# Performance work log

Measured on AMD Instinct MI355X. Metric: run time of the kernel, lower is better.

Reference implementation:

```python
import jax, jax.numpy as jnp
import numpy as np

B_SZ = 32; CTX = 8192; NP = 512; P = 16          # batch, context, n_patches, patch_size
DM = 1024; DS = 16; DC = 4; EXP = 2               # d_model, d_state, d_conv, expand
DI = EXP * DM                                     # d_inner = 2048
DTR = DM // 16                                    # dt_rank = 64


def _ln(x, g, b, eps=1e-5):
    m = x.mean(-1, keepdims=True)
    v = ((x - m) ** 2).mean(-1, keepdims=True)
    return (x - m) / jnp.sqrt(v + eps) * g + b


def _posemb_sincos_1d(n, d, temperature=10000.0):
    pos = jnp.arange(n, dtype=jnp.float32)
    omega = jnp.arange(d // 2, dtype=jnp.float32) / (d // 2 - 1)
    omega = 1.0 / (temperature ** omega)
    ang = pos[:, None] * omega[None, :]            # [n, d/2]
    return jnp.concatenate([jnp.sin(ang), jnp.cos(ang)], axis=1)  # [n, d]


def setup_inputs() -> dict:
    key = jax.random.key(0)
    ks = jax.random.split(key, 10)
    s = lambda k, shape, scale: jax.random.normal(k, shape, jnp.float32) * scale
    return {
        "x": jax.random.normal(ks[0], (B_SZ, CTX), jnp.float32),
        # patch embedding: LN(patch) -> Linear(P, DM) -> LN(DM)
        "ln1_g": jnp.ones((P,), jnp.float32), "ln1_b": jnp.zeros((P,), jnp.float32),
        "Wp": s(ks[1], (P, DM), P ** -0.5), "bp": jnp.zeros((DM,), jnp.float32),
        "ln2_g": jnp.ones((DM,), jnp.float32), "ln2_b": jnp.zeros((DM,), jnp.float32),
        # Mamba block params (mamba-ssm conventions: in_proj/out_proj bias=False, conv bias=True)
        "W_in": s(ks[2], (DM, 2 * DI), DM ** -0.5),
        "conv_w": s(ks[3], (DI, DC), DC ** -0.5), "conv_b": jnp.zeros((DI,), jnp.float32),
        "W_x": s(ks[4], (DI, DTR + 2 * DS), DI ** -0.5),
        "W_dt": s(ks[5], (DTR, DI), DTR ** -0.5),
        "b_dt": jnp.full((DI,), -4.6, jnp.float32),  # softplus(b_dt) ~ 0.01 (typical dt init)
        "A_log": jnp.log(jnp.broadcast_to(jnp.arange(1, DS + 1, dtype=jnp.float32), (DI, DS))),
        "D": jnp.ones((DI,), jnp.float32),
        "W_out": s(ks[6], (DI, DM), DI ** -0.5),
        "ln3_g": jnp.ones((DM,), jnp.float32), "ln3_b": jnp.zeros((DM,), jnp.float32),
        "Wh": s(ks[7], (DM, 1), DM ** -0.5), "bh": jnp.zeros((1,), jnp.float32),
    }


def reference(x, ln1_g, ln1_b, Wp, bp, ln2_g, ln2_b, W_in, conv_w, conv_b,
              W_x, W_dt, b_dt, A_log, D, W_out, ln3_g, ln3_b, Wh, bh):
    B = x.shape[0]
    # --- patch embedding: 'b 1 (n p) -> b n p' (c=1), LN, Linear, LN ---
    patches = x.reshape(B, NP, P)
    h = _ln(patches, ln1_g, ln1_b)
    h = h @ Wp + bp
    h = _ln(h, ln2_g, ln2_b)                        # [B, NP, DM]
    h = h + _posemb_sincos_1d(NP, DM)
    # --- Mamba block ---
    xz = h @ W_in                                   # [B, NP, 2*DI]
    u, z = jnp.split(xz, 2, axis=-1)                # [B, NP, DI] each
    # causal depthwise conv1d (kernel DC, left-padded), then SiLU
    up = jnp.pad(u, ((0, 0), (DC - 1, 0), (0, 0)))
    uc = sum(up[:, k:k + NP, :] * conv_w[:, k] for k in range(DC)) + conv_b
    uc = jax.nn.silu(uc)
    # input-dependent SSM params
    xd = uc @ W_x                                   # [B, NP, DTR+2*DS]
    dt, Bm, Cm = jnp.split(xd, [DTR, DTR + DS], axis=-1)
    delta = jax.nn.softplus(dt @ W_dt + b_dt)       # [B, NP, DI]
    A = -jnp.exp(A_log)                             # [DI, DS]

    def step(hstate, inps):
        d_t, B_t, C_t, u_t = inps                   # [B,DI], [B,DS], [B,DS], [B,DI]
        dA = jnp.exp(d_t[..., None] * A)            # [B, DI, DS]
        hstate = hstate * dA + (d_t * u_t)[..., None] * B_t[:, None, :]
        y_t = jnp.einsum('bdn,bn->bd', hstate, C_t)
        return hstate, y_t

    h0 = jnp.zeros((B, DI, DS), x.dtype)
    xs = (delta.transpose(1, 0, 2), Bm.transpose(1, 0, 2),
          Cm.transpose(1, 0, 2), uc.transpose(1, 0, 2))
    _, ys = jax.lax.scan(step, h0, xs)              # ys: [NP, B, DI]
    y = ys.transpose(1, 0, 2) + uc * D              # skip connection D*u
    y = y * jax.nn.silu(z)                          # gate
    y = y @ W_out                                   # [B, NP, DM]
    pooled = y.mean(axis=1)                         # [B, DM]
    out = (_ln(pooled, ln3_g, ln3_b) @ Wh + bh).squeeze()  # [B]
    return out
```

## Files before the change

### kernel.cpp

```cpp
#include <hip/hip_runtime.h>
#include <hip/hip_bf16.h>

#define BSZ  32
#define CTX  8192
#define NP_  512
#define PSZ  16
#define DM_  1024
#define DS_  16
#define DI_  2048
#define DTR_ 64
#define NTOK (BSZ*NP_)

typedef __hip_bfloat16 bf16;
typedef short bf16x8 __attribute__((ext_vector_type(8)));
typedef float f32x4  __attribute__((ext_vector_type(4)));

typedef __attribute__((address_space(3))) void lds_t;
typedef __attribute__((address_space(1))) void gbl_t;

__device__ inline float bf2f(bf16 v){ return __bfloat162float(v); }
__device__ inline bf16  f2bf(float v){ return __float2bfloat16(v); }
__device__ inline float bfs2f(short s){ union{unsigned u; float f;} x; x.u = ((unsigned)(unsigned short)s)<<16; return x.f; }
__device__ inline short f2bfs(float v){ bf16 b = f2bf(v); return *reinterpret_cast<short*>(&b); }
__device__ inline float fast_sigmoid(float x){ return 1.0f/(1.0f+__expf(-x)); }
__device__ inline void stout(float* p, float v){ *p = v; }
__device__ inline void stout(bf16* p, float v){ *p = f2bf(v); }
__device__ inline float hw_exp2(float x){ float r; asm("v_exp_f32 %0, %1" : "=v"(r) : "v"(x)); return r; }
__device__ inline float hw_log2(float x){ float r; asm("v_log_f32 %0, %1" : "=v"(r) : "v"(x)); return r; }
__device__ inline float softplus_fast(float x){
  if (x > 15.0f) return x;
  return 0.69314718f * hw_log2(1.0f + hw_exp2(x * 1.44269504f));
}

__device__ inline void gload_lds16(const void* g, void* l){
  __builtin_amdgcn_global_load_lds((const gbl_t*)g, (lds_t*)l, 16, 0, 0);
}

__global__ __launch_bounds__(256) void k_posemb(float* __restrict__ pe){
  int idx = blockIdx.x*256 + threadIdx.x;
  int n = idx >> 10, c = idx & 1023;
  int j2 = c & 511;
  float omega = exp2f(-13.2877123795495f * ((float)j2 * (1.0f/511.0f)));
  float ang = (float)n * omega;
  pe[idx] = (c < 512) ? sinf(ang) : cosf(ang);
}

__global__ __launch_bounds__(256) void k_transpose_cvt(
    const float* __restrict__ W, bf16* __restrict__ T,
    int ldw, int col0, int nvalid, int K)
{
  __shared__ float tile[64][65];
  int tid = threadIdx.x;
  int kb = blockIdx.x << 6, nb = blockIdx.y << 6;
  int c = tid & 63, r4 = tid >> 6;
  #pragma unroll
  for (int i=0;i<16;i++){
    int r = r4 + i*4;
    int kk = kb + r, nn = nb + c;
    float v = 0.f;
    if (kk < K && nn < nvalid) v = W[(size_t)kk*ldw + col0 + nn];
    tile[r][c] = v;
  }
  __syncthreads();
  #pragma unroll
  for (int i=0;i<16;i++){
    int r = r4 + i*4;
    T[(size_t)(nb + r)*K + kb + c] = f2bf(tile[c][r]);
  }
}

__global__ __launch_bounds__(256) void k_prep_cw(const float* __restrict__ cw, float* __restrict__ cwT){
  int idx = blockIdx.x*256 + threadIdx.x;
  int k = idx >> 11, d = idx & 2047;
  cwT[idx] = cw[d*4 + k];
}

__global__ __launch_bounds__(256) void k_patch(
    const float* __restrict__ x, const float* __restrict__ g1, const float* __restrict__ b1,
    const float* __restrict__ Wp, const float* __restrict__ bp,
    const float* __restrict__ g2, const float* __restrict__ b2,
    const float* __restrict__ pe, bf16* __restrict__ h)
{
  __shared__ float pns[2][16];
  __shared__ float red[8];
  int tid = threadIdx.x;
  int w = tid >> 6, l = tid & 63;
  int tok0 = blockIdx.x << 4;
  int bb = tok0 >> 9, n0 = tok0 & 511;
  float wreg[4][16];
  #pragma unroll
  for (int q=0;q<4;q++)
    #pragma unroll
    for (int i=0;i<16;i++)
      wreg[q][i] = Wp[i*1024 + tid + q*256];
  float bpv[4], g2v[4], b2v[4];
  #pragma unroll
  for (int q=0;q<4;q++){
    int j = tid + q*256;
    bpv[q] = bp[j]; g2v[q] = g2[j]; b2v[q] = b2[j];
  }
  float g1v = 0.f, b1v = 0.f;
  if (tid < 16){ g1v = g1[tid]; b1v = b1[tid]; }
  for (int tt=0; tt<16; ++tt){
    int buf = tt & 1;
    if (tid < 16){
      float v = x[(size_t)bb*CTX + (n0+tt)*16 + tid];
      float m = v;
      #pragma unroll
      for (int o=1;o<16;o<<=1) m += __shfl_xor(m, o, 64);
      m *= (1.0f/16.0f);
      float dv = v - m;
      float s = dv*dv;
      #pragma unroll
      for (int o=1;o<16;o<<=1) s += __shfl_xor(s, o, 64);
      float rs = rsqrtf(s*(1.0f/16.0f) + 1e-5f);
      pns[buf][tid] = dv*rs*g1v + b1v;
    }
    __syncthreads();
    float acc[4];
    #pragma unroll
    for (int q=0;q<4;q++) acc[q] = bpv[q];
    #pragma unroll
    for (int i=0;i<16;i++){
      float p = pns[buf][i];
      #pragma unroll
      for (int q=0;q<4;q++) acc[q] += p*wreg[q][i];
    }
    float s1 = acc[0]+acc[1]+acc[2]+acc[3];
    float s2 = acc[0]*acc[0]+acc[1]*acc[1]+acc[2]*acc[2]+acc[3]*acc[3];
    #pragma unroll
    for (int o=32;o;o>>=1){ s1 += __shfl_down(s1,o,64); s2 += __shfl_down(s2,o,64); }
    if (l==0){ red[w]=s1; red[4+w]=s2; }
    __syncthreads();
    float mu  = (red[0]+red[1]+red[2]+red[3])*(1.0f/1024.0f);
    float var = (red[4]+red[5]+red[6]+red[7])*(1.0f/1024.0f) - mu*mu;
    float rs2 = rsqrtf(var + 1e-5f);
    size_t tok = (size_t)(tok0 + tt);
    #pragma unroll
    for (int q=0;q<4;q++){
      int j = tid + q*256;
      float val = (acc[q]-mu)*rs2*g2v[q] + b2v[q] + pe[(n0+tt)*1024 + j];
      h[tok*1024 + j] = f2bf(val);
    }
  }
}

__global__ __launch_bounds__(512, 2) void k_gemm256(
    const bf16* __restrict__ A, const bf16* __restrict__ BT,
    bf16* __restrict__ Cu, bf16* __restrict__ Cz, int M, int N, int K)
{
  __shared__ __align__(16) bf16 As[2][256*64];
  __shared__ __align__(16) bf16 Bs[2][256*64];
  const int tid = threadIdx.x;
  const int w = tid >> 6, l = tid & 63, lr = l & 15, lg = l >> 4;
  const int wm = w >> 2, wn = w & 3;
  int nblk = N >> 8;
  int nwg = gridDim.x;
  int wg  = (blockIdx.x & 7) * (nwg >> 3) + (blockIdx.x >> 3);
  const int GM = 4;
  int band = GM * nblk;
  int grp = wg / band, loc = wg % band;
  int bm = grp*GM + (loc % GM);
  int bn = loc / GM;
  int m0 = bm << 8, n0 = bn << 8;

  f32x4 acc[8][4] = {};

  int rowS[4], colS[4];
  #pragma unroll
  for (int j=0;j<4;j++){
    int bo = (j*8 + w)*1024 + l*16;
    int r = bo >> 7;
    int c = (bo & 127) ^ ((r & 7) << 4);
    rowS[j] = r; colS[j] = c >> 1;
  }
  const bf16* Ag = A  + (size_t)m0 * K;
  const bf16* Bg = BT + (size_t)n0 * K;

  #define STAGE(buf, kt) do {                                                   \
    _Pragma("unroll")                                                           \
    for (int j=0;j<4;j++)                                                       \
      gload_lds16(Ag + (size_t)rowS[j]*K + (kt) + colS[j], &As[buf][(j*8+w)*512]); \
    _Pragma("unroll")                                                           \
    for (int j=0;j<4;j++)                                                       \
      gload_lds16(Bg + (size_t)rowS[j]*K + (kt) + colS[j], &Bs[buf][(j*8+w)*512]); \
  } while(0)

  int cswz[2];
  cswz[0] = (lg*8) ^ ((lr&7)<<3);
  cswz[1] = (32 + lg*8) ^ ((lr&7)<<3);
  const int rbA = (wm*128 + lr) * 64;
  const int rbB = (wn*64  + lr) * 64;

  #define COMPUTE(buf) do {                                                     \
    _Pragma("unroll")                                                           \
    for (int q=0;q<4;q++){                                                      \
      const int kk = q >> 1, rh = q & 1;                                        \
      bf16x8 af[4], bq[4];                                                      \
      _Pragma("unroll")                                                         \
      for (int i=0;i<4;i++) af[i] = *(const bf16x8*)&As[buf][rbA + (rh*4+i)*1024 + cswz[kk]]; \
      _Pragma("unroll")                                                         \
      for (int j=0;j<4;j++) bq[j] = *(const bf16x8*)&Bs[buf][rbB + j*1024 + cswz[kk]]; \
      __builtin_amdgcn_s_setprio(1);                                            \
      _Pragma("unroll")                                                         \
      for (int i=0;i<4;i++)                                                     \
        _Pragma("unroll")                                                       \
        for (int j=0;j<4;j++)                                                   \
          acc[rh*4+i][j] = __builtin_amdgcn_mfma_f32_16x16x32_bf16(af[i], bq[j], acc[rh*4+i][j], 0,0,0); \
      __builtin_amdgcn_s_setprio(0);                                            \
    }                                                                           \
  } while(0)

  STAGE(0, 0);
  STAGE(1, 64);
  const int NT2 = K >> 7;
  int kt = 0;
  for (int t=0; t<NT2; ++t){
    const bool last = (t == NT2-1);
    asm volatile("s_waitcnt vmcnt(8)" ::: "memory");
    __builtin_amdgcn_sched_barrier(0);
    asm volatile("s_barrier" ::: "memory");
    COMPUTE(0);
    asm volatile("s_barrier" ::: "memory");
    __builtin_amdgcn_sched_barrier(0);
    if (!last) STAGE(0, kt + 128);
    if (!last) { asm volatile("s_waitcnt vmcnt(8)" ::: "memory"); }
    else       { asm volatile("s_waitcnt vmcnt(0)" ::: "memory"); }
    __builtin_amdgcn_sched_barrier(0);
    asm volatile("s_barrier" ::: "memory");
    COMPUTE(1);
    if (!last){
      asm volatile("s_barrier" ::: "memory");
      __builtin_amdgcn_sched_barrier(0);
      STAGE(1, kt + 192);
    }
    kt += 128;
  }
  #undef STAGE
  #undef COMPUTE

  #pragma unroll
  for (int fr=0;fr<8;fr++)
    #pragma unroll
    for (int fc=0;fc<4;fc++)
      #pragma unroll
      for (int rr=0;rr<4;rr++){
        int row  = m0 + wm*128 + fr*16 + lg*4 + rr;
        int gcol = n0 + wn*64 + fc*16 + lr;
        float v = acc[fr][fc][rr];
        if (gcol < 2048) Cu[(size_t)row*2048 + gcol] = f2bf(v);
        else { v = v * fast_sigmoid(v); Cz[(size_t)row*2048 + gcol - 2048] = f2bf(v); }
      }
}

template<int EPI, typename OT>
__global__ __launch_bounds__(256) void k_gemm_bt(
    const bf16* __restrict__ A, const bf16* __restrict__ BT, OT* __restrict__ C,
    bf16* __restrict__ C2, int M, int N, int K, const float* __restrict__ bias)
{
  __shared__ __align__(16) bf16 As[128*32];
  __shared__ __align__(16) bf16 Bs[128*32];
  int tid = threadIdx.x;
  int mblk = M >> 7, nblk = N >> 7;
  int nwg = gridDim.x;
  int wg  = (blockIdx.x & 7) * (nwg >> 3) + (blockIdx.x >> 3);
  const int GM = 8;
  int band = GM * nblk;
  int grp = wg / band, loc = wg % band;
  int bm = grp*GM + (loc % GM);
  int bn = loc / GM;
  int m0 = bm << 7, n0 = bn << 7;
  int w = tid >> 6, l = tid & 63, lr = l & 15, lg = l >> 4;
  int wm = w >> 1, wn = w & 1;
  f32x4 acc[4][4] = {};
  int r0 = tid >> 2, c0 = (tid & 3) << 3;
  const bf16* Asrc = A  + (size_t)(m0 + r0) * K + c0;
  const bf16* Bsrc = BT + (size_t)(n0 + r0) * K + c0;
  bf16* AsW = As + w*512;
  bf16* BsW = Bs + w*512;
  for (int kt = 0; kt < K; kt += 32){
    __syncthreads();
    gload_lds16(Asrc + kt,                   AsW);
    gload_lds16(Asrc + (size_t)64*K + kt,    AsW + 2048);
    gload_lds16(Bsrc + kt,                   BsW);
    gload_lds16(Bsrc + (size_t)64*K + kt,    BsW + 2048);
    __syncthreads();
    bf16x8 af[4], bfr[4];
    #pragma unroll
    for (int i=0;i<4;i++) af[i]  = *(const bf16x8*)(As + (wm*64 + i*16 + lr)*32 + lg*8);
    #pragma unroll
    for (int j=0;j<4;j++) bfr[j] = *(const bf16x8*)(Bs + (wn*64 + j*16 + lr)*32 + lg*8);
    #pragma unroll
    for (int i=0;i<4;i++)
      #pragma unroll
      for (int j=0;j<4;j++)
        acc[i][j] = __builtin_amdgcn_mfma_f32_16x16x32_bf16(af[i], bfr[j], acc[i][j], 0,0,0);
  }
  #pragma unroll
  for (int i=0;i<4;i++)
    #pragma unroll
    for (int j=0;j<4;j++)
      #pragma unroll
      for (int r=0;r<4;r++){
        int row = m0 + wm*64 + i*16 + lg*4 + r;
        int col = wn*64 + j*16 + lr;
        int gcol = n0 + col;
        float v = acc[i][j][r];
        if (EPI == 0) stout(&C[(size_t)row*N + gcol], v);
        if (EPI == 1){ v = softplus_fast(v + bias[gcol]); stout(&C[(size_t)row*N + gcol], v); }
      }
}

__global__ __launch_bounds__(256) void k_gemm_xk(
    const bf16* __restrict__ A, const bf16* __restrict__ BT,
    float* __restrict__ C0, float* __restrict__ C1)
{
  __shared__ __align__(16) bf16 As[128*32];
  __shared__ __align__(16) bf16 Bs[128*32];
  int tid = threadIdx.x;
  int nwg = gridDim.x;
  int wg  = (blockIdx.x & 7) * (nwg >> 3) + (blockIdx.x >> 3);
  int chunk = wg >> 7;
  int bm = wg & 127;
  int m0 = bm << 7;
  int w = tid >> 6, l = tid & 63, lr = l & 15, lg = l >> 4;
  int wm = w >> 1, wn = w & 1;
  f32x4 acc[4][4] = {};
  int r0 = tid >> 2, c0 = (tid & 3) << 3;
  const bf16* Asrc = A  + (size_t)(m0 + r0) * 2048 + chunk*1024 + c0;
  const bf16* Bsrc = BT + (size_t)r0 * 2048 + chunk*1024 + c0;
  bf16* AsW = As + w*512;
  bf16* BsW = Bs + w*512;
  float* Cp = chunk ? C1 : C0;
  for (int kt = 0; kt < 1024; kt += 32){
    __syncthreads();
    gload_lds16(Asrc + kt,                      AsW);
    gload_lds16(Asrc + (size_t)64*2048 + kt,    AsW + 2048);
    gload_lds16(Bsrc + kt,                      BsW);
    gload_lds16(Bsrc + (size_t)64*2048 + kt,    BsW + 2048);
    __syncthreads();
    bf16x8 af[4], bfr[4];
    #pragma unroll
    for (int i=0;i<4;i++) af[i]  = *(const bf16x8*)(As + (wm*64 + i*16 + lr)*32 + lg*8);
    #pragma unroll
    for (int j=0;j<4;j++) bfr[j] = *(const bf16x8*)(Bs + (wn*64 + j*16 + lr)*32 + lg*8);
    #pragma unroll
    for (int i=0;i<4;i++)
      #pragma unroll
      for (int j=0;j<4;j++)
        acc[i][j] = __builtin_amdgcn_mfma_f32_16x16x32_bf16(af[i], bfr[j], acc[i][j], 0,0,0);
  }
  #pragma unroll
  for (int i=0;i<4;i++)
    #pragma unroll
    for (int j=0;j<4;j++)
      #pragma unroll
      for (int r=0;r<4;r++){
        int row = m0 + wm*64 + i*16 + lg*4 + r;
        int gcol = wn*64 + j*16 + lr;
        Cp[(size_t)row*128 + gcol] = acc[i][j][r];
      }
}

__global__ __launch_bounds__(256) void k_xproj_fix(
    float* __restrict__ xd, const float* __restrict__ p1, bf16* __restrict__ dt)
{
  int idx = blockIdx.x*256 + threadIdx.x;
  int row = idx >> 7, col = idx & 127;
  float v = xd[idx] + p1[idx];
  xd[idx] = v;
  if (col < 64) dt[(row << 6) + col] = f2bf(v);
}

__global__ __launch_bounds__(256) void k_conv(
    const bf16* __restrict__ u, const float* __restrict__ cwT, const float* __restrict__ cb,
    bf16* __restrict__ uc)
{
  int tid = threadIdx.x;
  int d = tid << 3;
  int tok0 = blockIdx.x << 4;
  int n0 = tok0 & 511;
  float wk[4][8];
  #pragma unroll
  for (int k=0;k<4;k++){
    *(float4*)&wk[k][0] = *(const float4*)(cwT + k*2048 + d);
    *(float4*)&wk[k][4] = *(const float4*)(cwT + k*2048 + d + 4);
  }
  float cbv[8];
  *(float4*)&cbv[0] = *(const float4*)(cb + d);
  *(float4*)&cbv[4] = *(const float4*)(cb + d + 4);
  bf16x8 w0, w1, w2;
  if (n0 == 0){
    w0 = (bf16x8){0,0,0,0,0,0,0,0}; w1 = w0; w2 = w0;
  } else {
    w0 = *(const bf16x8*)(u + (size_t)(tok0-3)*2048 + d);
    w1 = *(const bf16x8*)(u + (size_t)(tok0-2)*2048 + d);
    w2 = *(const bf16x8*)(u + (size_t)(tok0-1)*2048 + d);
  }
  #pragma unroll 4
  for (int t=0; t<16; ++t){
    size_t tok = (size_t)(tok0 + t);
    bf16x8 cur = *(const bf16x8*)(u + tok*2048 + d);
    bf16x8 res;
    #pragma unroll
    for (int j=0;j<8;j++){
      float a = cbv[j]
              + wk[0][j]*bfs2f(w0[j]) + wk[1][j]*bfs2f(w1[j])
              + wk[2][j]*bfs2f(w2[j]) + wk[3][j]*bfs2f(cur[j]);
      res[j] = f2bfs(a * fast_sigmoid(a));
    }
    *(bf16x8*)(uc + tok*2048 + d) = res;
    w0 = w1; w1 = w2; w2 = cur;
  }
}

__global__ __launch_bounds__(256) void k_scan(
    const bf16* __restrict__ delta, const bf16* __restrict__ uc, const bf16* __restrict__ g,
    const float* __restrict__ xd, const float* __restrict__ A_log,
    const float* __restrict__ Dp, float* __restrict__ ysum)
{
  int tid = threadIdx.x;
  int q  = tid & 3;
  int dl = tid >> 2;
  int b  = blockIdx.x >> 5;
  int d  = ((blockIdx.x & 31) << 6) + dl;
  const float L2E = 1.44269504f;
  float4 t4 = *(const float4*)(A_log + (size_t)d*16 + q*4);
  float An0 = -__expf(t4.x)*L2E, An1 = -__expf(t4.y)*L2E,
        An2 = -__expf(t4.z)*L2E, An3 = -__expf(t4.w)*L2E;
  float Dd = (q == 0) ? Dp[d] : 0.0f;
  float h0=0.f,h1=0.f,h2=0.f,h3=0.f;
  float acc = 0.0f;
  unsigned o1 = (unsigned)b*1048576u + (unsigned)d;
  unsigned o2 = (unsigned)b*16384u + 16u + (unsigned)q;
  const float4* __restrict__ x4 = (const float4*)xd;
  #pragma unroll 4
  for (int t=0; t<512; ++t){
    float dt = bf2f(delta[o1]);
    float ut = bf2f(uc[o1]);
    float gt = bf2f(g[o1]);
    float4 Bq = x4[o2];
    float4 Cq = x4[o2 + 4u];
    o1 += 2048u; o2 += 32u;
    float du = dt*ut;
    float y;
    float e0 = hw_exp2(dt*An0); h0 = h0*e0 + du*Bq.x; y  = h0*Cq.x;
    float e1 = hw_exp2(dt*An1); h1 = h1*e1 + du*Bq.y; y += h1*Cq.y;
    float e2 = hw_exp2(dt*An2); h2 = h2*e2 + du*Bq.z; y += h2*Cq.z;
    float e3 = hw_exp2(dt*An3); h3 = h3*e3 + du*Bq.w; y += h3*Cq.w;
    acc += (y + ut*Dd) * gt;
  }
  acc += __shfl_xor(acc, 1, 64);
  acc += __shfl_xor(acc, 2, 64);
  if (q == 0) ysum[(size_t)b*2048 + d] = acc;
}

__global__ __launch_bounds__(256) void k_poolgemm_part(
    const float* __restrict__ ysum, const float* __restrict__ Wo, float* __restrict__ partial)
{
  __shared__ float ys[32][64];
  int tid = threadIdx.x;
  int jb = blockIdx.x & 15;
  int kc = blockIdx.x >> 4;
  int j  = jb*64 + (tid & 63);
  int b0 = tid >> 6;
  #pragma unroll
  for (int i=0;i<8;i++){
    int e = tid + i*256;
    int bb = e >> 6, kk = e & 63;
    ys[bb][kk] = ysum[(size_t)bb*2048 + kc*64 + kk];
  }
  __syncthreads();
  float acc[8];
  #pragma unroll
  for (int p=0;p<8;p++) acc[p] = 0.f;
  #pragma unroll 4
  for (int kk=0;kk<64;kk++){
    float wv = Wo[(size_t)(kc*64 + kk)*1024 + j];
    #pragma unroll
    for (int p=0;p<8;p++) acc[p] += ys[b0*8 + p][kk] * wv;
  }
  #pragma unroll
  for (int p=0;p<8;p++)
    partial[((size_t)kc*32 + b0*8 + p)*1024 + j] = acc[p];
}

__global__ __launch_bounds__(256) void k_pool_reduce(
    const float* __restrict__ partial, float* __restrict__ pooled)
{
  int idx = blockIdx.x*256 + threadIdx.x;
  float s = 0.f;
  #pragma unroll 8
  for (int kc=0;kc<32;kc++) s += partial[(size_t)kc*32768 + idx];
  pooled[idx] = s * (1.0f/512.0f);
}

__global__ __launch_bounds__(256) void k_head(
    const float* __restrict__ pooled, const float* __restrict__ g, const float* __restrict__ bb,
    const float* __restrict__ Wh, const float* __restrict__ bh, float* __restrict__ out)
{
  __shared__ float red[8];
  int b = blockIdx.x, tid = threadIdx.x;
  float v[4];
  #pragma unroll
  for (int q=0;q<4;q++) v[q] = pooled[(size_t)b*1024 + tid + q*256];
  float s1 = v[0]+v[1]+v[2]+v[3];
  float s2 = v[0]*v[0]+v[1]*v[1]+v[2]*v[2]+v[3]*v[3];
  #pragma unroll
  for (int o=32;o;o>>=1){ s1 += __shfl_down(s1,o,64); s2 += __shfl_down(s2,o,64); }
  int w = tid>>6, l = tid&63;
  if (l==0){ red[w]=s1; red[4+w]=s2; }
  __syncthreads();
  float mu  = (red[0]+red[1]+red[2]+red[3])*(1.0f/1024.0f);
  float var = (red[4]+red[5]+red[6]+red[7])*(1.0f/1024.0f) - mu*mu;
  float rs = rsqrtf(var + 1e-5f);
  float p = 0.f;
  #pragma unroll
  for (int q=0;q<4;q++){
    int jv = tid + q*256;
    p += ((v[q]-mu)*rs*g[jv] + bb[jv]) * Wh[jv];
  }
  #pragma unroll
  for (int o=32;o;o>>=1) p += __shfl_down(p,o,64);
  __syncthreads();
  if (l==0) red[w] = p;
  __syncthreads();
  if (tid==0) out[b] = red[0]+red[1]+red[2]+red[3] + bh[0];
}

extern "C" void kernel_launch(void* const* d_in, const int* in_sizes, int n_in,
                              void* d_out, int out_size, void* d_ws, size_t ws_size,
                              hipStream_t stream)
{
  const float* x     = (const float*)d_in[0];
  const float* ln1_g = (const float*)d_in[1];
  const float* ln1_b = (const float*)d_in[2];
  const float* Wp    = (const float*)d_in[3];
  const float* bp    = (const float*)d_in[4];
  const float* ln2_g = (const float*)d_in[5];
  const float* ln2_b = (const float*)d_in[6];
  const float* W_in  = (const float*)d_in[7];
  const float* conv_w= (const float*)d_in[8];
  const float* conv_b= (const float*)d_in[9];
  const float* W_x   = (const float*)d_in[10];
  const float* W_dt  = (const float*)d_in[11];
  const float* b_dt  = (const float*)d_in[12];
  const float* A_log = (const float*)d_in[13];
  const float* Dv    = (const float*)d_in[14];
  const float* W_out = (const float*)d_in[15];
  const float* ln3_g = (const float*)d_in[16];
  const float* ln3_b = (const float*)d_in[17];
  const float* Wh    = (const float*)d_in[18];
  const float* bh    = (const float*)d_in[19];

  char* ws = (char*)d_ws;
  size_t o = 0;
  bf16*  u_delta = (bf16*)(ws + o); o += (size_t)NTOK*DI_*2;
  bf16*  zbuf    = (bf16*)(ws + o); o += (size_t)NTOK*DI_*2;
  bf16*  ucbuf   = (bf16*)(ws + o); o += (size_t)NTOK*DI_*2;
  char*  poolA   = (ws + o);        o += (size_t)NTOK*DM_*2;
  bf16*  winT    = (bf16*)(ws + o); o += (size_t)2*DI_*DM_*2;
  float* pe      = (float*)(ws + o); o += (size_t)NP_*DM_*4;
  bf16*  hbuf    = (bf16*)poolA;
  float* xdbuf   = (float*)(poolA + 0);
  bf16*  dtbuf   = (bf16*) (poolA + 8388608);
  bf16*  wxT     = (bf16*) (poolA + 10485760);
  bf16*  wdtT    = (bf16*) (poolA + 11010048);
  float* ysumbuf = (float*)(poolA + 11272192);
  float* pooledb = (float*)(poolA + 11534336);
  float* partial = (float*)(poolA + 12582912);
  float* cwT     = (float*)(poolA + 16777216);
  float* xpart1  = (float*)winT;

  k_posemb        <<<2048, 256, 0, stream>>>(pe);
  k_patch         <<<1024, 256, 0, stream>>>(x, ln1_g, ln1_b, Wp, bp, ln2_g, ln2_b, pe, hbuf);
  k_transpose_cvt <<<dim3(16,64),256,0,stream>>>(W_in, winT, 4096, 0, 4096, 1024);
  k_gemm256       <<<1024, 512, 0, stream>>>(hbuf, winT, u_delta, zbuf, NTOK, 4096, 1024);
  k_prep_cw       <<<32,   256, 0, stream>>>(conv_w, cwT);
  k_conv          <<<1024, 256, 0, stream>>>(u_delta, cwT, conv_b, ucbuf);
  k_transpose_cvt <<<dim3(32,2),256,0,stream>>>(W_x, wxT, 96, 0, 96, 2048);
  k_gemm_xk       <<<256,  256, 0, stream>>>(ucbuf, wxT, xdbuf, xpart1);
  k_xproj_fix     <<<8192, 256, 0, stream>>>(xdbuf, xpart1, dtbuf);
  k_transpose_cvt <<<dim3(1,32),256,0,stream>>>(W_dt, wdtT, 2048, 0, 2048, 64);
  k_gemm_bt<1,bf16><<<2048,256, 0, stream>>>(dtbuf, wdtT, u_delta, nullptr, NTOK, 2048, 64, b_dt);
  k_scan          <<<1024, 256, 0, stream>>>(u_delta, ucbuf, zbuf, xdbuf, A_log, Dv, ysumbuf);
  k_poolgemm_part <<<512,  256, 0, stream>>>(ysumbuf, W_out, partial);
  k_pool_reduce   <<<128,  256, 0, stream>>>(partial, pooledb);
  k_head          <<<32,   256, 0, stream>>>(pooledb, ln3_g, ln3_b, Wh, bh, (float*)d_out);
  (void)in_sizes; (void)n_in; (void)out_size; (void)ws_size;
}
```

Baseline: 505.6 us.

## Merge weight-prep kernels, split x-proj GEMM K four ways, reorder MFMA fragment loads

Five small setup kernels (positional embedding, three weight transposes, conv weight transpose) become one launch that dispatches on block index, which cuts launch count and serialization. The x-projection GEMM is split into four K chunks instead of two, doubling its grid from 256 to 512 blocks for better CU occupancy. The partials go into buffers reused from u_delta and are summed in the fix-up kernel, which adds extra memory traffic. The big GEMM's inner loop now loads each B fragment once per k-step instead of twice, which reduces LDS reads.

```diff
diff --git a/kernel.cpp b/kernel.cpp
--- a/kernel.cpp
+++ b/kernel.cpp
@@ -36,22 +36,11 @@
   __builtin_amdgcn_global_load_lds((const gbl_t*)g, (lds_t*)l, 16, 0, 0);
 }
 
-__global__ __launch_bounds__(256) void k_posemb(float* __restrict__ pe){
-  int idx = blockIdx.x*256 + threadIdx.x;
-  int n = idx >> 10, c = idx & 1023;
-  int j2 = c & 511;
-  float omega = exp2f(-13.2877123795495f * ((float)j2 * (1.0f/511.0f)));
-  float ang = (float)n * omega;
-  pe[idx] = (c < 512) ? sinf(ang) : cosf(ang);
-}
-
-__global__ __launch_bounds__(256) void k_transpose_cvt(
-    const float* __restrict__ W, bf16* __restrict__ T,
-    int ldw, int col0, int nvalid, int K)
-{
-  __shared__ float tile[64][65];
-  int tid = threadIdx.x;
-  int kb = blockIdx.x << 6, nb = blockIdx.y << 6;
+__device__ inline void transpose_cvt_body(
+    int bx, int by, const float* __restrict__ W, bf16* __restrict__ T,
+    int ldw, int col0, int nvalid, int K, int tid, float (*tile)[65])
+{
+  int kb = bx << 6, nb = by << 6;
   int c = tid & 63, r4 = tid >> 6;
   #pragma unroll
   for (int i=0;i<16;i++){
@@ -69,10 +58,35 @@
   }
 }
 
-__global__ __launch_bounds__(256) void k_prep_cw(const float* __restrict__ cw, float* __restrict__ cwT){
-  int idx = blockIdx.x*256 + threadIdx.x;
-  int k = idx >> 11, d = idx & 2047;
-  cwT[idx] = cw[d*4 + k];
+__global__ __launch_bounds__(256) void k_prep_all(
+    const float* __restrict__ W_in, bf16* __restrict__ winT,
+    const float* __restrict__ W_x,  bf16* __restrict__ wxT,
+    const float* __restrict__ W_dt, bf16* __restrict__ wdtT,
+    float* __restrict__ pe,
+    const float* __restrict__ cw, float* __restrict__ cwT)
+{
+  __shared__ float tile[64][65];
+  int b = blockIdx.x, tid = threadIdx.x;
+  if (b < 1024){
+    transpose_cvt_body(b & 15, b >> 4, W_in, winT, 4096, 0, 4096, 1024, tid, tile);
+  } else if (b < 1088){
+    int t = b - 1024;
+    transpose_cvt_body(t & 31, t >> 5, W_x, wxT, 96, 0, 96, 2048, tid, tile);
+  } else if (b < 1120){
+    int t = b - 1088;
+    transpose_cvt_body(0, t, W_dt, wdtT, 2048, 0, 2048, 64, tid, tile);
+  } else if (b < 3168){
+    int idx = (b - 1120)*256 + tid;
+    int n = idx >> 10, c = idx & 1023;
+    int j2 = c & 511;
+    float omega = exp2f(-13.2877123795495f * ((float)j2 * (1.0f/511.0f)));
+    float ang = (float)n * omega;
+    pe[idx] = (c < 512) ? sinf(ang) : cosf(ang);
+  } else {
+    int idx = (b - 3168)*256 + tid;
+    int k = idx >> 11, d = idx & 2047;
+    cwT[idx] = cw[d*4 + k];
+  }
 }
 
 __global__ __launch_bounds__(256) void k_patch(
@@ -194,20 +208,23 @@
 
   #define COMPUTE(buf) do {                                                     \
     _Pragma("unroll")                                                           \
-    for (int q=0;q<4;q++){                                                      \
-      const int kk = q >> 1, rh = q & 1;                                        \
-      bf16x8 af[4], bq[4];                                                      \
-      _Pragma("unroll")                                                         \
-      for (int i=0;i<4;i++) af[i] = *(const bf16x8*)&As[buf][rbA + (rh*4+i)*1024 + cswz[kk]]; \
+    for (int kk=0;kk<2;kk++){                                                   \
+      bf16x8 bq[4];                                                             \
       _Pragma("unroll")                                                         \
       for (int j=0;j<4;j++) bq[j] = *(const bf16x8*)&Bs[buf][rbB + j*1024 + cswz[kk]]; \
-      __builtin_amdgcn_s_setprio(1);                                            \
       _Pragma("unroll")                                                         \
-      for (int i=0;i<4;i++)                                                     \
+      for (int rh=0;rh<2;rh++){                                                 \
+        bf16x8 af[4];                                                           \
         _Pragma("unroll")                                                       \
-        for (int j=0;j<4;j++)                                                   \
-          acc[rh*4+i][j] = __builtin_amdgcn_mfma_f32_16x16x32_bf16(af[i], bq[j], acc[rh*4+i][j], 0,0,0); \
-      __builtin_amdgcn_s_setprio(0);                                            \
+        for (int i=0;i<4;i++) af[i] = *(const bf16x8*)&As[buf][rbA + (rh*4+i)*1024 + cswz[kk]]; \
+        __builtin_amdgcn_s_setprio(1);                                          \
+        _Pragma("unroll")                                                       \
+        for (int i=0;i<4;i++)                                                   \
+          _Pragma("unroll")                                                     \
+          for (int j=0;j<4;j++)                                                 \
+            acc[rh*4+i][j] = __builtin_amdgcn_mfma_f32_16x16x32_bf16(af[i], bq[j], acc[rh*4+i][j], 0,0,0); \
+        __builtin_amdgcn_s_setprio(0);                                          \
+      }                                                                         \
     }                                                                           \
   } while(0)
 
@@ -313,7 +330,8 @@
 
 __global__ __launch_bounds__(256) void k_gemm_xk(
     const bf16* __restrict__ A, const bf16* __restrict__ BT,
-    float* __restrict__ C0, float* __restrict__ C1)
+    float* __restrict__ C0, float* __restrict__ C1,
+    float* __restrict__ C2, float* __restrict__ C3)
 {
   __shared__ __align__(16) bf16 As[128*32];
   __shared__ __align__(16) bf16 Bs[128*32];
@@ -323,16 +341,17 @@
   int chunk = wg >> 7;
   int bm = wg & 127;
   int m0 = bm << 7;
+  int kbase = chunk << 9;
   int w = tid >> 6, l = tid & 63, lr = l & 15, lg = l >> 4;
   int wm = w >> 1, wn = w & 1;
   f32x4 acc[4][4] = {};
   int r0 = tid >> 2, c0 = (tid & 3) << 3;
-  const bf16* Asrc = A  + (size_t)(m0 + r0) * 2048 + chunk*1024 + c0;
-  const bf16* Bsrc = BT + (size_t)r0 * 2048 + chunk*1024 + c0;
+  const bf16* Asrc = A  + (size_t)(m0 + r0) * 2048 + kbase + c0;
+  const bf16* Bsrc = BT + (size_t)r0 * 2048 + kbase + c0;
   bf16* AsW = As + w*512;
   bf16* BsW = Bs + w*512;
-  float* Cp = chunk ? C1 : C0;
-  for (int kt = 0; kt < 1024; kt += 32){
+  float* Cp = (chunk==0) ? C0 : (chunk==1) ? C1 : (chunk==2) ? C2 : C3;
+  for (int kt = 0; kt < 512; kt += 32){
     __syncthreads();
     gload_lds16(Asrc + kt,                      AsW);
     gload_lds16(Asrc + (size_t)64*2048 + kt,    AsW + 2048);
@@ -363,11 +382,13 @@
 }
 
 __global__ __launch_bounds__(256) void k_xproj_fix(
-    float* __restrict__ xd, const float* __restrict__ p1, bf16* __restrict__ dt)
+    float* __restrict__ xd, const float* __restrict__ p1,
+    const float* __restrict__ p2, const float* __restrict__ p3,
+    bf16* __restrict__ dt)
 {
   int idx = blockIdx.x*256 + threadIdx.x;
   int row = idx >> 7, col = idx & 127;
-  float v = xd[idx] + p1[idx];
+  float v = xd[idx] + p1[idx] + p2[idx] + p3[idx];
   xd[idx] = v;
   if (col < 64) dt[(row << 6) + col] = f2bf(v);
 }
@@ -561,27 +582,25 @@
   char*  poolA   = (ws + o);        o += (size_t)NTOK*DM_*2;
   bf16*  winT    = (bf16*)(ws + o); o += (size_t)2*DI_*DM_*2;
   float* pe      = (float*)(ws + o); o += (size_t)NP_*DM_*4;
+  bf16*  wxT     = (bf16*)(ws + o); o += (size_t)128*2048*2;
+  bf16*  wdtT    = (bf16*)(ws + o); o += (size_t)2048*64*2;
+  float* cwT     = (float*)(ws + o); o += (size_t)4*2048*4;
   bf16*  hbuf    = (bf16*)poolA;
   float* xdbuf   = (float*)(poolA + 0);
   bf16*  dtbuf   = (bf16*) (poolA + 8388608);
-  bf16*  wxT     = (bf16*) (poolA + 10485760);
-  bf16*  wdtT    = (bf16*) (poolA + 11010048);
   float* ysumbuf = (float*)(poolA + 11272192);
   float* pooledb = (float*)(poolA + 11534336);
   float* partial = (float*)(poolA + 12582912);
-  float* cwT     = (float*)(poolA + 16777216);
   float* xpart1  = (float*)winT;
-
-  k_posemb        <<<2048, 256, 0, stream>>>(pe);
+  float* xpart2  = (float*)u_delta;
+  float* xpart3  = (float*)((char*)u_delta + 8388608);
+
+  k_prep_all      <<<3200, 256, 0, stream>>>(W_in, winT, W_x, wxT, W_dt, wdtT, pe, conv_w, cwT);
   k_patch         <<<1024, 256, 0, stream>>>(x, ln1_g, ln1_b, Wp, bp, ln2_g, ln2_b, pe, hbuf);
-  k_transpose_cvt <<<dim3(16,64),256,0,stream>>>(W_in, winT, 4096, 0, 4096, 1024);
   k_gemm256       <<<1024, 512, 0, stream>>>(hbuf, winT, u_delta, zbuf, NTOK, 4096, 1024);
-  k_prep_cw       <<<32,   256, 0, stream>>>(conv_w, cwT);
   k_conv          <<<1024, 256, 0, stream>>>(u_delta, cwT, conv_b, ucbuf);
-  k_transpose_cvt <<<dim3(32,2),256,0,stream>>>(W_x, wxT, 96, 0, 96, 2048);
-  k_gemm_xk       <<<256,  256, 0, stream>>>(ucbuf, wxT, xdbuf, xpart1);
-  k_xproj_fix     <<<8192, 256, 0, stream>>>(xdbuf, xpart1, dtbuf);
-  k_transpose_cvt <<<dim3(1,32),256,0,stream>>>(W_dt, wdtT, 2048, 0, 2048, 64);
+  k_gemm_xk       <<<512,  256, 0, stream>>>(ucbuf, wxT, xdbuf, xpart1, xpart2, xpart3);
+  k_xproj_fix     <<<8192, 256, 0, stream>>>(xdbuf, xpart1, xpart2, xpart3, dtbuf);
   k_gemm_bt<1,bf16><<<2048,256, 0, stream>>>(dtbuf, wdtT, u_delta, nullptr, NTOK, 2048, 64, b_dt);
   k_scan          <<<1024, 256, 0, stream>>>(u_delta, ucbuf, zbuf, xdbuf, A_log, Dv, ysumbuf);
   k_poolgemm_part <<<512,  256, 0, stream>>>(ysumbuf, W_out, partial);
```

Measured after the change: 476.8 us. -5.7%, faster.
